# Performance work log

Hardware: AMD Instinct MI355X
Metric: run time of the kernel (lower is better)

The kernel has to match this reference:

```python
import jax, jax.numpy as jnp
import numpy as np

MORA_DIV = 2


def setup_inputs() -> dict:
    key = jax.random.key(0)
    k1, k2, k3, k4 = jax.random.split(key, 4)
    d = 4096
    m = d // MORA_DIV
    x = jax.random.normal(k1, (4, 2048, d), dtype=jnp.float32)
    weight = jax.random.normal(k2, (d, d), dtype=jnp.float32) * 0.02
    mora = jax.random.normal(k3, (m, m), dtype=jnp.float32) * 0.02
    # dora_mag initialized as column L2 norm of the frozen weight (1, d_in)
    dora_mag = jnp.linalg.norm(weight, axis=0, keepdims=True)
    return {"x": x, "weight": weight, "mora": mora, "dora_mag": dora_mag}


def reference(x, weight, mora, dora_mag):
    # Tile the small adapter into full (d_out, d_in): repeat_interleave on both dims
    adapter = jnp.repeat(jnp.repeat(mora, MORA_DIV, axis=0), MORA_DIV, axis=1)
    w = weight + adapter                      # (d_out, d_in)
    col_norm = jnp.linalg.norm(w, axis=0, keepdims=True)  # (1, d_in)
    w = dora_mag * (w / col_norm)             # DoRA magnitude rescale
    return jnp.einsum('bsd,od->bso', x, w)    # F.linear, no bias
```

## Files before the change

kernel.cpp:

```cpp
#include <hip/hip_runtime.h>
#include <stdint.h>

#define M_TOT 8192
#define N_TOT 4096
#define K_TOT 4096
#define BM 256
#define BN 256
#define BK 32
#define NT (K_TOT / BK)

typedef short  s16x8 __attribute__((ext_vector_type(8)));
typedef unsigned short u16x8 __attribute__((ext_vector_type(8)));
typedef float  f32x4 __attribute__((ext_vector_type(4)));

__device__ __forceinline__ unsigned short f32_to_bf16(float f) {
  union { float f; unsigned u; } v; v.f = f;
  unsigned r = v.u + 0x7FFFu + ((v.u >> 16) & 1u);
  return (unsigned short)(r >> 16);
}

__device__ __forceinline__ void gload_lds16(void* lds, const void* g) {
  __builtin_amdgcn_global_load_lds(
      (const __attribute__((address_space(1))) unsigned int*)g,
      (__attribute__((address_space(3))) unsigned int*)lds,
      16, 0, 0);
}

__global__ void colnorm_partial_k(const float* __restrict__ weight,
                                  const float* __restrict__ mora,
                                  float* __restrict__ partials) {
  int d = blockIdx.x * 256 + threadIdx.x;
  int o0 = blockIdx.y * 128;
  float s = 0.f;
  #pragma unroll 4
  for (int o = o0; o < o0 + 128; ++o) {
    float w = weight[(size_t)o * K_TOT + d] + mora[(size_t)(o >> 1) * 2048 + (d >> 1)];
    s = fmaf(w, w, s);
  }
  partials[blockIdx.y * K_TOT + d] = s;
}

__global__ void scale_k(const float* __restrict__ partials,
                        const float* __restrict__ dora_mag,
                        float* __restrict__ scale) {
  int d = blockIdx.x * 256 + threadIdx.x;
  float s = 0.f;
  #pragma unroll
  for (int c = 0; c < 32; ++c) s += partials[c * K_TOT + d];
  scale[d] = dora_mag[d] / sqrtf(s);
}

__global__ void pack_w_k(const float* __restrict__ weight,
                         const float* __restrict__ mora,
                         const float* __restrict__ scale,
                         unsigned short* __restrict__ wb) {
  size_t idx = ((size_t)blockIdx.x * 256 + threadIdx.x) * 8;
  int o = (int)(idx >> 12);
  int d = (int)(idx & (K_TOT - 1));
  float4 w0 = *(const float4*)(weight + idx);
  float4 w1 = *(const float4*)(weight + idx + 4);
  float4 mv = *(const float4*)(mora + (size_t)(o >> 1) * 2048 + (d >> 1));
  float4 s0 = *(const float4*)(scale + d);
  float4 s1 = *(const float4*)(scale + d + 4);
  u16x8 r;
  r[0] = f32_to_bf16((w0.x + mv.x) * s0.x);
  r[1] = f32_to_bf16((w0.y + mv.x) * s0.y);
  r[2] = f32_to_bf16((w0.z + mv.y) * s0.z);
  r[3] = f32_to_bf16((w0.w + mv.y) * s0.w);
  r[4] = f32_to_bf16((w1.x + mv.z) * s1.x);
  r[5] = f32_to_bf16((w1.y + mv.z) * s1.y);
  r[6] = f32_to_bf16((w1.z + mv.w) * s1.z);
  r[7] = f32_to_bf16((w1.w + mv.w) * s1.w);
  *(u16x8*)(wb + idx) = r;
}

__global__ void pack_x_k(const float* __restrict__ x, unsigned short* __restrict__ xb) {
  size_t idx = ((size_t)blockIdx.x * 256 + threadIdx.x) * 8;
  float4 v0 = *(const float4*)(x + idx);
  float4 v1 = *(const float4*)(x + idx + 4);
  u16x8 r;
  r[0] = f32_to_bf16(v0.x); r[1] = f32_to_bf16(v0.y);
  r[2] = f32_to_bf16(v0.z); r[3] = f32_to_bf16(v0.w);
  r[4] = f32_to_bf16(v1.x); r[5] = f32_to_bf16(v1.y);
  r[6] = f32_to_bf16(v1.z); r[7] = f32_to_bf16(v1.w);
  *(u16x8*)(xb + idx) = r;
}

__device__ __forceinline__ void stage_tile(
    const unsigned short* ga0, const unsigned short* ga1,
    const unsigned short* gb0, const unsigned short* gb1,
    short* la, short* lb, int lo0, int lo1, int kt) {
  gload_lds16(la + lo0, ga0 + kt);
  gload_lds16(lb + lo0, gb0 + kt);
  gload_lds16(la + lo1, ga1 + kt);
  gload_lds16(lb + lo1, gb1 + kt);
}

__device__ __forceinline__ void compute_tile(
    const short* la, const short* lb, int aoff, int boff, f32x4 (&acc)[8][4]) {
  s16x8 bfr[4], afr[8];
  #pragma unroll
  for (int n = 0; n < 4; ++n)
    bfr[n] = *(const s16x8*)(lb + boff + n * 16 * BK);
  #pragma unroll
  for (int m = 0; m < 8; ++m)
    afr[m] = *(const s16x8*)(la + aoff + m * 16 * BK);
  __builtin_amdgcn_s_setprio(1);
  #pragma unroll
  for (int m = 0; m < 8; ++m)
    #pragma unroll
    for (int n = 0; n < 4; ++n)
      acc[m][n] = __builtin_amdgcn_mfma_f32_16x16x32_bf16(afr[m], bfr[n], acc[m][n], 0, 0, 0);
  __builtin_amdgcn_s_setprio(0);
}

__global__ void __launch_bounds__(512, 2) gemm_bf16_k(
    const unsigned short* __restrict__ xb,
    const unsigned short* __restrict__ wb,
    float* __restrict__ out) {
  __shared__ short lds[4][2][BM * BK];

  const int tid = threadIdx.x;
  const int l   = tid & 63;
  const int wid = tid >> 6;
  const int wm  = wid >> 2;
  const int wn  = wid & 3;

  const int orig = blockIdx.x;
  const int swz  = (orig & 7) * (512 >> 3) + (orig >> 3);
  const int by = swz >> 4;
  const int bx = swz & 15;

  const unsigned short* ag = xb + (size_t)(by * BM) * K_TOT;
  const unsigned short* bg = wb + (size_t)(bx * BN) * K_TOT;

  const int c0 = tid, c1 = 512 + tid;
  const unsigned short* ga0 = ag + (size_t)(c0 >> 2) * K_TOT + (c0 & 3) * 8;
  const unsigned short* ga1 = ag + (size_t)(c1 >> 2) * K_TOT + (c1 & 3) * 8;
  const unsigned short* gb0 = bg + (size_t)(c0 >> 2) * K_TOT + (c0 & 3) * 8;
  const unsigned short* gb1 = bg + (size_t)(c1 >> 2) * K_TOT + (c1 & 3) * 8;
  const int lo0 = (tid & ~63) * 8;
  const int lo1 = (512 + (tid & ~63)) * 8;

  const int lrow = l & 15;
  const int lko  = (l >> 4) * 8;
  const int aoff = (wm * 128 + lrow) * BK + lko;
  const int boff = (wn * 64  + lrow) * BK + lko;

  f32x4 acc[8][4] = {};

  #define STG(t) stage_tile(ga0, ga1, gb0, gb1, lds[(t) & 3][0], lds[(t) & 3][1], lo0, lo1, (t) * BK)
  #define CMP(t) compute_tile(lds[(t) & 3][0], lds[(t) & 3][1], aoff, boff, acc)

  STG(0); STG(1); STG(2);

  #pragma unroll 1
  for (int t = 0; t < NT - 3; ++t) {
    asm volatile("s_waitcnt vmcnt(8)" ::: "memory");
    __builtin_amdgcn_s_barrier();
    STG(t + 3);
    CMP(t);
  }
  asm volatile("s_waitcnt vmcnt(8)" ::: "memory");
  __builtin_amdgcn_s_barrier();
  CMP(NT - 3);
  asm volatile("s_waitcnt vmcnt(4)" ::: "memory");
  __builtin_amdgcn_s_barrier();
  CMP(NT - 2);
  asm volatile("s_waitcnt vmcnt(0)" ::: "memory");
  __builtin_amdgcn_s_barrier();
  CMP(NT - 1);

  #undef STG
  #undef CMP

  const int row0 = by * BM + wm * 128 + (l >> 4) * 4;
  const int col0 = bx * BN + wn * 64 + lrow;
  #pragma unroll
  for (int m = 0; m < 8; ++m)
    #pragma unroll
    for (int n = 0; n < 4; ++n) {
      #pragma unroll
      for (int j = 0; j < 4; ++j)
        out[(size_t)(row0 + m * 16 + j) * N_TOT + col0 + n * 16] = acc[m][n][j];
    }
}

__global__ void gemm_fb_k(const float* __restrict__ x, const float* __restrict__ weight,
                          const float* __restrict__ mora, const float* __restrict__ scale,
                          float* __restrict__ out) {
  __shared__ float As[64][17];
  __shared__ float Bs[64][17];
  int t = threadIdx.x;
  int bx = blockIdx.x, by = blockIdx.y;
  int tr = t >> 4, tc = t & 15;
  float c[4][4] = {};
  for (int kt = 0; kt < K_TOT; kt += 16) {
    #pragma unroll
    for (int r = 0; r < 4; ++r) {
      int idx = r * 256 + t;
      int row = idx >> 4, col = idx & 15;
      As[row][col] = x[(size_t)(by * 64 + row) * K_TOT + kt + col];
      int o = bx * 64 + row, d = kt + col;
      Bs[row][col] = (weight[(size_t)o * K_TOT + d] + mora[(size_t)(o >> 1) * 2048 + (d >> 1)]) * scale[d];
    }
    __syncthreads();
    #pragma unroll
    for (int k = 0; k < 16; ++k) {
      float av[4], bv[4];
      #pragma unroll
      for (int i = 0; i < 4; ++i) av[i] = As[tr * 4 + i][k];
      #pragma unroll
      for (int j = 0; j < 4; ++j) bv[j] = Bs[tc * 4 + j][k];
      #pragma unroll
      for (int i = 0; i < 4; ++i)
        #pragma unroll
        for (int j = 0; j < 4; ++j)
          c[i][j] = fmaf(av[i], bv[j], c[i][j]);
    }
    __syncthreads();
  }
  #pragma unroll
  for (int i = 0; i < 4; ++i)
    #pragma unroll
    for (int j = 0; j < 4; ++j)
      out[(size_t)(by * 64 + tr * 4 + i) * N_TOT + bx * 64 + tc * 4 + j] = c[i][j];
}

extern "C" void kernel_launch(void* const* d_in, const int* in_sizes, int n_in,
                              void* d_out, int out_size, void* d_ws, size_t ws_size,
                              hipStream_t stream) {
  const float* x      = (const float*)d_in[0];
  const float* weight = (const float*)d_in[1];
  const float* mora   = (const float*)d_in[2];
  const float* dora   = (const float*)d_in[3];
  float* out = (float*)d_out;

  char* ws = (char*)d_ws;
  float* partials = (float*)ws;
  float* scale    = (float*)(ws + (512 << 10));
  const size_t OFF_W = (size_t)1 << 20;
  unsigned short* wbuf = (unsigned short*)(ws + OFF_W);
  unsigned short* xbuf = (unsigned short*)(ws + OFF_W + (size_t)N_TOT * K_TOT * 2);
  const size_t NEED = OFF_W + (size_t)N_TOT * K_TOT * 2 + (size_t)M_TOT * K_TOT * 2;

  dim3 b256(256);
  colnorm_partial_k<<<dim3(16, 32), b256, 0, stream>>>(weight, mora, partials);
  scale_k<<<16, b256, 0, stream>>>(partials, dora, scale);

  if (ws_size >= NEED) {
    pack_w_k<<<(N_TOT * K_TOT) / (256 * 8), b256, 0, stream>>>(weight, mora, scale, wbuf);
    pack_x_k<<<(M_TOT * K_TOT) / (256 * 8), b256, 0, stream>>>(x, xbuf);
    gemm_bf16_k<<<(M_TOT / BM) * (N_TOT / BN), 512, 0, stream>>>(xbuf, wbuf, out);
  } else {
    gemm_fb_k<<<dim3(N_TOT / 64, M_TOT / 64), b256, 0, stream>>>(x, weight, mora, scale, out);
  }
}
```

Measured before the change: 338.5 us.

## Split GEMM main loop into half-tile phases interleaving LDS reads, loads and MFMA

Restructures the bf16 GEMM main loop into a ping-pong style schedule. Each K tile is processed in two halves of four A fragments, and the global-to-LDS loads for A and B are issued between the halves. Extra barriers and explicit lgkmcnt waits sit between the phases. This cuts A-fragment register use from 8 to 4 and is meant to overlap LDS reads and global loads with MFMA more evenly. The cost is many more barriers per tile, which may add synchronisation stalls.

```diff
diff --git a/kernel.cpp b/kernel.cpp
--- a/kernel.cpp
+++ b/kernel.cpp
@@ -86,34 +86,6 @@
   *(u16x8*)(xb + idx) = r;
 }
 
-__device__ __forceinline__ void stage_tile(
-    const unsigned short* ga0, const unsigned short* ga1,
-    const unsigned short* gb0, const unsigned short* gb1,
-    short* la, short* lb, int lo0, int lo1, int kt) {
-  gload_lds16(la + lo0, ga0 + kt);
-  gload_lds16(lb + lo0, gb0 + kt);
-  gload_lds16(la + lo1, ga1 + kt);
-  gload_lds16(lb + lo1, gb1 + kt);
-}
-
-__device__ __forceinline__ void compute_tile(
-    const short* la, const short* lb, int aoff, int boff, f32x4 (&acc)[8][4]) {
-  s16x8 bfr[4], afr[8];
-  #pragma unroll
-  for (int n = 0; n < 4; ++n)
-    bfr[n] = *(const s16x8*)(lb + boff + n * 16 * BK);
-  #pragma unroll
-  for (int m = 0; m < 8; ++m)
-    afr[m] = *(const s16x8*)(la + aoff + m * 16 * BK);
-  __builtin_amdgcn_s_setprio(1);
-  #pragma unroll
-  for (int m = 0; m < 8; ++m)
-    #pragma unroll
-    for (int n = 0; n < 4; ++n)
-      acc[m][n] = __builtin_amdgcn_mfma_f32_16x16x32_bf16(afr[m], bfr[n], acc[m][n], 0, 0, 0);
-  __builtin_amdgcn_s_setprio(0);
-}
-
 __global__ void __launch_bounds__(512, 2) gemm_bf16_k(
     const unsigned short* __restrict__ xb,
     const unsigned short* __restrict__ wb,
@@ -135,44 +107,92 @@
   const unsigned short* bg = wb + (size_t)(bx * BN) * K_TOT;
 
   const int c0 = tid, c1 = 512 + tid;
-  const unsigned short* ga0 = ag + (size_t)(c0 >> 2) * K_TOT + (c0 & 3) * 8;
-  const unsigned short* ga1 = ag + (size_t)(c1 >> 2) * K_TOT + (c1 & 3) * 8;
-  const unsigned short* gb0 = bg + (size_t)(c0 >> 2) * K_TOT + (c0 & 3) * 8;
-  const unsigned short* gb1 = bg + (size_t)(c1 >> 2) * K_TOT + (c1 & 3) * 8;
+  const unsigned short* gA0 = ag + (size_t)(c0 >> 2) * K_TOT + (c0 & 3) * 8;
+  const unsigned short* gA1 = ag + (size_t)(c1 >> 2) * K_TOT + (c1 & 3) * 8;
+  const unsigned short* gB0 = bg + (size_t)(c0 >> 2) * K_TOT + (c0 & 3) * 8;
+  const unsigned short* gB1 = bg + (size_t)(c1 >> 2) * K_TOT + (c1 & 3) * 8;
   const int lo0 = (tid & ~63) * 8;
-  const int lo1 = (512 + (tid & ~63)) * 8;
+  const int lo1 = lo0 + 512 * 8;
 
   const int lrow = l & 15;
   const int lko  = (l >> 4) * 8;
-  const int aoff = (wm * 128 + lrow) * BK + lko;
-  const int boff = (wn * 64  + lrow) * BK + lko;
-
+  const int aoffb = (wm * 128 + lrow) * BK + lko;
+  const int boffb = (wn * 64  + lrow) * BK + lko;
+
+  s16x8 afr[4], bfr[4];
   f32x4 acc[8][4] = {};
 
-  #define STG(t) stage_tile(ga0, ga1, gb0, gb1, lds[(t) & 3][0], lds[(t) & 3][1], lo0, lo1, (t) * BK)
-  #define CMP(t) compute_tile(lds[(t) & 3][0], lds[(t) & 3][1], aoff, boff, acc)
-
-  STG(0); STG(1); STG(2);
+#define STG_A(t) { short* p = &lds[(t) & 3][0][0]; \
+    gload_lds16(p + lo0, gA0 + (size_t)(t) * BK); \
+    gload_lds16(p + lo1, gA1 + (size_t)(t) * BK); }
+#define STG_B(t) { short* p = &lds[(t) & 3][1][0]; \
+    gload_lds16(p + lo0, gB0 + (size_t)(t) * BK); \
+    gload_lds16(p + lo1, gB1 + (size_t)(t) * BK); }
+#define DS_A(t, mb) { const short* p = &lds[(t) & 3][0][aoffb + (mb) * 16 * BK]; \
+    afr[0] = *(const s16x8*)(p);               afr[1] = *(const s16x8*)(p + 16 * BK); \
+    afr[2] = *(const s16x8*)(p + 32 * BK);     afr[3] = *(const s16x8*)(p + 48 * BK); }
+#define DS_B(t) { const short* p = &lds[(t) & 3][1][boffb]; \
+    bfr[0] = *(const s16x8*)(p);               bfr[1] = *(const s16x8*)(p + 16 * BK); \
+    bfr[2] = *(const s16x8*)(p + 32 * BK);     bfr[3] = *(const s16x8*)(p + 48 * BK); }
+#define BAR() __builtin_amdgcn_s_barrier()
+#define LGKM0() asm volatile("s_waitcnt lgkmcnt(0)" ::: "memory")
+#define VM8() asm volatile("s_waitcnt vmcnt(8)" ::: "memory")
+#define VM4() asm volatile("s_waitcnt vmcnt(4)" ::: "memory")
+#define VM0() asm volatile("s_waitcnt vmcnt(0)" ::: "memory")
+#define MM(mb) { __builtin_amdgcn_s_setprio(1); \
+    _Pragma("unroll") for (int mm = 0; mm < 4; ++mm) { \
+      _Pragma("unroll") for (int nn = 0; nn < 4; ++nn) \
+        acc[(mb) + mm][nn] = __builtin_amdgcn_mfma_f32_16x16x32_bf16(afr[mm], bfr[nn], acc[(mb) + mm][nn], 0, 0, 0); } \
+    __builtin_amdgcn_s_setprio(0); }
+
+  STG_A(0); STG_B(0); STG_A(1); STG_B(1); STG_A(2); STG_B(2);
+  VM8(); BAR();
 
   #pragma unroll 1
-  for (int t = 0; t < NT - 3; ++t) {
-    asm volatile("s_waitcnt vmcnt(8)" ::: "memory");
-    __builtin_amdgcn_s_barrier();
-    STG(t + 3);
-    CMP(t);
-  }
-  asm volatile("s_waitcnt vmcnt(8)" ::: "memory");
-  __builtin_amdgcn_s_barrier();
-  CMP(NT - 3);
-  asm volatile("s_waitcnt vmcnt(4)" ::: "memory");
-  __builtin_amdgcn_s_barrier();
-  CMP(NT - 2);
-  asm volatile("s_waitcnt vmcnt(0)" ::: "memory");
-  __builtin_amdgcn_s_barrier();
-  CMP(NT - 1);
-
-  #undef STG
-  #undef CMP
+  for (int t = 0; t < NT - 4; t += 2) {
+    DS_A(t, 0); DS_B(t);
+    STG_A(t + 3);
+    BAR(); LGKM0(); MM(0); BAR();
+    DS_A(t, 4);
+    STG_B(t + 3);
+    BAR(); LGKM0(); MM(4);
+    VM8(); BAR();
+    DS_A(t + 1, 0); DS_B(t + 1);
+    STG_A(t + 4);
+    BAR(); LGKM0(); MM(0); BAR();
+    DS_A(t + 1, 4);
+    STG_B(t + 4);
+    BAR(); LGKM0(); MM(4);
+    VM8(); BAR();
+  }
+
+  DS_A(124, 0); DS_B(124);
+  STG_A(127);
+  BAR(); LGKM0(); MM(0); BAR();
+  DS_A(124, 4);
+  STG_B(127);
+  BAR(); LGKM0(); MM(4);
+  VM8(); BAR();
+  DS_A(125, 0); DS_B(125);
+  BAR(); LGKM0(); MM(0); BAR();
+  DS_A(125, 4);
+  BAR(); LGKM0(); MM(4);
+  VM4(); BAR();
+  DS_A(126, 0); DS_B(126);
+  BAR(); LGKM0(); MM(0); BAR();
+  DS_A(126, 4);
+  BAR(); LGKM0(); MM(4);
+  VM0(); BAR();
+  DS_A(127, 0); DS_B(127);
+  BAR(); LGKM0(); MM(0); BAR();
+  DS_A(127, 4);
+  LGKM0(); MM(4);
+
+#undef STG_A
+#undef STG_B
+#undef DS_A
+#undef DS_B
+#undef MM
 
   const int row0 = by * BM + wm * 128 + (l >> 4) * 4;
   const int col0 = bx * BN + wn * 64 + lrow;
```

Result: no change. 336.3 us (-0.6%).

## Restructure bf16 GEMM main loop into 8-phase ping-pong schedule with swizzled LDS

Applied to the files above, without the earlier changes.

Replaces the 4-stage BK=32 pipeline with a double-buffered BK=64 schedule. Each K step is split into quarter-tile MFMA phases that interleave LDS fragment reads, global-to-LDS stages and barriers. An XOR swizzle on the 16-byte chunk index is applied to both the global load layout and the LDS reads to avoid bank conflicts. The aim is finer overlap of memory traffic with MFMA and fewer LDS conflicts, at the cost of many more barriers per iteration and a more fragile hand-scheduled sequence.

```diff
diff --git a/kernel.cpp b/kernel.cpp
--- a/kernel.cpp
+++ b/kernel.cpp
@@ -6,8 +6,8 @@
 #define K_TOT 4096
 #define BM 256
 #define BN 256
-#define BK 32
-#define NT (K_TOT / BK)
+#define BK 64
+#define NIT (K_TOT / (2 * BK))
 
 typedef short  s16x8 __attribute__((ext_vector_type(8)));
 typedef unsigned short u16x8 __attribute__((ext_vector_type(8)));
@@ -86,45 +86,18 @@
   *(u16x8*)(xb + idx) = r;
 }
 
-__device__ __forceinline__ void stage_tile(
-    const unsigned short* ga0, const unsigned short* ga1,
-    const unsigned short* gb0, const unsigned short* gb1,
-    short* la, short* lb, int lo0, int lo1, int kt) {
-  gload_lds16(la + lo0, ga0 + kt);
-  gload_lds16(lb + lo0, gb0 + kt);
-  gload_lds16(la + lo1, ga1 + kt);
-  gload_lds16(lb + lo1, gb1 + kt);
-}
-
-__device__ __forceinline__ void compute_tile(
-    const short* la, const short* lb, int aoff, int boff, f32x4 (&acc)[8][4]) {
-  s16x8 bfr[4], afr[8];
-  #pragma unroll
-  for (int n = 0; n < 4; ++n)
-    bfr[n] = *(const s16x8*)(lb + boff + n * 16 * BK);
-  #pragma unroll
-  for (int m = 0; m < 8; ++m)
-    afr[m] = *(const s16x8*)(la + aoff + m * 16 * BK);
-  __builtin_amdgcn_s_setprio(1);
-  #pragma unroll
-  for (int m = 0; m < 8; ++m)
-    #pragma unroll
-    for (int n = 0; n < 4; ++n)
-      acc[m][n] = __builtin_amdgcn_mfma_f32_16x16x32_bf16(afr[m], bfr[n], acc[m][n], 0, 0, 0);
-  __builtin_amdgcn_s_setprio(0);
-}
-
 __global__ void __launch_bounds__(512, 2) gemm_bf16_k(
     const unsigned short* __restrict__ xb,
     const unsigned short* __restrict__ wb,
     float* __restrict__ out) {
-  __shared__ short lds[4][2][BM * BK];
+  __shared__ short lds[2][2][2][128 * 64];
 
   const int tid = threadIdx.x;
   const int l   = tid & 63;
   const int wid = tid >> 6;
   const int wm  = wid >> 2;
   const int wn  = wid & 3;
+  const int wnh = wn >> 1;
 
   const int orig = blockIdx.x;
   const int swz  = (orig & 7) * (512 >> 3) + (orig >> 3);
@@ -134,55 +107,101 @@
   const unsigned short* ag = xb + (size_t)(by * BM) * K_TOT;
   const unsigned short* bg = wb + (size_t)(bx * BN) * K_TOT;
 
-  const int c0 = tid, c1 = 512 + tid;
-  const unsigned short* ga0 = ag + (size_t)(c0 >> 2) * K_TOT + (c0 & 3) * 8;
-  const unsigned short* ga1 = ag + (size_t)(c1 >> 2) * K_TOT + (c1 & 3) * 8;
-  const unsigned short* gb0 = bg + (size_t)(c0 >> 2) * K_TOT + (c0 & 3) * 8;
-  const unsigned short* gb1 = bg + (size_t)(c1 >> 2) * K_TOT + (c1 & 3) * 8;
-  const int lo0 = (tid & ~63) * 8;
-  const int lo1 = (512 + (tid & ~63)) * 8;
+  const int row0 = tid >> 3;
+  const int kb0  = (tid & 7) ^ (row0 & 7);
+  const int off0 = row0 * K_TOT + kb0 * 8;
+  const int off1 = off0 + 64 * K_TOT;
+  const int ldst = (tid & ~63) * 8;
 
   const int lrow = l & 15;
-  const int lko  = (l >> 4) * 8;
-  const int aoff = (wm * 128 + lrow) * BK + lko;
-  const int boff = (wn * 64  + lrow) * BK + lko;
-
+  const int lq   = l >> 4;
+  const int key  = lrow & 7;
+  const int ab0  = lrow * 64 + ((lq) ^ key) * 8;
+  const int ab1  = lrow * 64 + ((4 + lq) ^ key) * 8;
+
+  s16x8 aA[4][2], bB[4][2];
   f32x4 acc[8][4] = {};
 
-  #define STG(t) stage_tile(ga0, ga1, gb0, gb1, lds[(t) & 3][0], lds[(t) & 3][1], lo0, lo1, (t) * BK)
-  #define CMP(t) compute_tile(lds[(t) & 3][0], lds[(t) & 3][1], aoff, boff, acc)
-
-  STG(0); STG(1); STG(2);
+#define STAGE(buf, op, h, t) { \
+    short* d = &lds[buf][op][h][0] + ldst; \
+    const unsigned short* s = ((op) ? bg : ag) + (size_t)(h) * 128 * K_TOT + (size_t)(t) * BK; \
+    gload_lds16(d, s + off0); \
+    gload_lds16(d + 4096, s + off1); }
+#define DSA(buf, mh) { const short* p = &lds[buf][0][wm][0]; \
+    _Pragma("unroll") for (int mm = 0; mm < 4; ++mm) { \
+      aA[mm][0] = *(const s16x8*)(p + ((mh) * 4 + mm) * 1024 + ab0); \
+      aA[mm][1] = *(const s16x8*)(p + ((mh) * 4 + mm) * 1024 + ab1); } }
+#define DSB(buf, nh) { const short* p = &lds[buf][1][wnh][0] + (wn & 1) * 4096; \
+    _Pragma("unroll") for (int nn = 0; nn < 2; ++nn) { \
+      bB[(nh) * 2 + nn][0] = *(const s16x8*)(p + ((nh) * 2 + nn) * 1024 + ab0); \
+      bB[(nh) * 2 + nn][1] = *(const s16x8*)(p + ((nh) * 2 + nn) * 1024 + ab1); } }
+#define MMQ(mh, nh) { __builtin_amdgcn_s_setprio(1); \
+    _Pragma("unroll") for (int mm = 0; mm < 4; ++mm) \
+      _Pragma("unroll") for (int nn = 0; nn < 2; ++nn) \
+        _Pragma("unroll") for (int kh = 0; kh < 2; ++kh) \
+          acc[(mh) * 4 + mm][(nh) * 2 + nn] = __builtin_amdgcn_mfma_f32_16x16x32_bf16( \
+              aA[mm][kh], bB[(nh) * 2 + nn][kh], acc[(mh) * 4 + mm][(nh) * 2 + nn], 0, 0, 0); \
+    __builtin_amdgcn_s_setprio(0); }
+#define BARm()  asm volatile("s_barrier" ::: "memory")
+#define LGKM0() asm volatile("s_waitcnt lgkmcnt(0)" ::: "memory")
+#define VM2()   asm volatile("s_waitcnt vmcnt(2)" ::: "memory")
+#define VM0()   asm volatile("s_waitcnt vmcnt(0)" ::: "memory")
+#define SB0()   __builtin_amdgcn_sched_barrier(0)
+
+  STAGE(0, 0, 0, 0); STAGE(0, 0, 1, 0); STAGE(0, 1, 0, 0); STAGE(0, 1, 1, 0);
+  STAGE(1, 0, 0, 1);
+  VM2(); BARm();
 
   #pragma unroll 1
-  for (int t = 0; t < NT - 3; ++t) {
-    asm volatile("s_waitcnt vmcnt(8)" ::: "memory");
-    __builtin_amdgcn_s_barrier();
-    STG(t + 3);
-    CMP(t);
-  }
-  asm volatile("s_waitcnt vmcnt(8)" ::: "memory");
-  __builtin_amdgcn_s_barrier();
-  CMP(NT - 3);
-  asm volatile("s_waitcnt vmcnt(4)" ::: "memory");
-  __builtin_amdgcn_s_barrier();
-  CMP(NT - 2);
-  asm volatile("s_waitcnt vmcnt(0)" ::: "memory");
-  __builtin_amdgcn_s_barrier();
-  CMP(NT - 1);
-
-  #undef STG
-  #undef CMP
-
-  const int row0 = by * BM + wm * 128 + (l >> 4) * 4;
-  const int col0 = bx * BN + wn * 64 + lrow;
+  for (int i = 0; i < NIT - 1; ++i) {
+    const int t1 = 2 * i + 1;
+    DSA(0, 0); DSB(0, 0); STAGE(1, 0, 1, t1);
+    BARm(); LGKM0(); SB0(); MMQ(0, 0); BARm();
+    DSB(0, 1); STAGE(1, 1, 0, t1);
+    BARm(); LGKM0(); SB0(); MMQ(0, 1); BARm();
+    DSA(0, 1); STAGE(1, 1, 1, t1);
+    BARm(); LGKM0(); SB0(); MMQ(1, 0); BARm();
+    STAGE(0, 0, 0, t1 + 1);
+    BARm(); LGKM0(); SB0(); MMQ(1, 1); VM2(); BARm();
+    DSA(1, 0); DSB(1, 0); STAGE(0, 0, 1, t1 + 1);
+    BARm(); LGKM0(); SB0(); MMQ(0, 0); BARm();
+    DSB(1, 1); STAGE(0, 1, 0, t1 + 1);
+    BARm(); LGKM0(); SB0(); MMQ(0, 1); BARm();
+    DSA(1, 1); STAGE(0, 1, 1, t1 + 1);
+    BARm(); LGKM0(); SB0(); MMQ(1, 0); BARm();
+    STAGE(1, 0, 0, t1 + 2);
+    BARm(); LGKM0(); SB0(); MMQ(1, 1); VM2(); BARm();
+  }
+
+  DSA(0, 0); DSB(0, 0); STAGE(1, 0, 1, 63);
+  BARm(); LGKM0(); SB0(); MMQ(0, 0); BARm();
+  DSB(0, 1); STAGE(1, 1, 0, 63);
+  BARm(); LGKM0(); SB0(); MMQ(0, 1); BARm();
+  DSA(0, 1); STAGE(1, 1, 1, 63);
+  BARm(); LGKM0(); SB0(); MMQ(1, 0); BARm();
+  BARm(); LGKM0(); SB0(); MMQ(1, 1); VM0(); BARm();
+  DSA(1, 0); DSB(1, 0);
+  BARm(); LGKM0(); SB0(); MMQ(0, 0); BARm();
+  DSB(1, 1);
+  BARm(); LGKM0(); SB0(); MMQ(0, 1); BARm();
+  DSA(1, 1);
+  BARm(); LGKM0(); SB0(); MMQ(1, 0); BARm();
+  LGKM0(); SB0(); MMQ(1, 1);
+
+#undef STAGE
+#undef DSA
+#undef DSB
+#undef MMQ
+
+  const int row0o = by * BM + wm * 128 + lq * 4;
+  const int col0o = bx * BN + wn * 64 + lrow;
   #pragma unroll
   for (int m = 0; m < 8; ++m)
     #pragma unroll
     for (int n = 0; n < 4; ++n) {
       #pragma unroll
       for (int j = 0; j < 4; ++j)
-        out[(size_t)(row0 + m * 16 + j) * N_TOT + col0 + n * 16] = acc[m][n][j];
+        out[(size_t)(row0o + m * 16 + j) * N_TOT + col0o + n * 16] = acc[m][n][j];
     }
 }
 
```

Result: faster. 307.5 us (-9.1%).
